# Kernel optimization log

Measured on AMD Instinct MI355X. Metric: run time of the kernel, lower is better.

The kernel has to match this reference:

```python
import jax, jax.numpy as jnp
import numpy as np

B, T, D = 2, 4096, 512
H = 8  # heads; head_dim = D // H = 64


def setup_inputs() -> dict:
    key = jax.random.key(0)
    ks = jax.random.split(key, 8)
    s = 0.02
    return {
        "queries": jax.random.normal(ks[0], (B, T, D), jnp.float32),
        "keys": jax.random.normal(ks[1], (B, T, D), jnp.float32),
        "values": jax.random.normal(ks[2], (B, T, D), jnp.float32),
        "Wq": jax.random.normal(ks[3], (D, D), jnp.float32) * s,
        "Wk": jax.random.normal(ks[4], (D, D), jnp.float32) * s,
        "Wv": jax.random.normal(ks[5], (D, D), jnp.float32) * s,
        "Wo": jax.random.normal(ks[6], (D, D), jnp.float32) * s,
        "bo": jnp.zeros((D,), jnp.float32),
    }


def reference(queries, keys, values, Wq, Wk, Wv, Wo, bo):
    # pad_dim = 0 for in_dim=512, n_heads=8, so no padding needed.
    Bq, Tq, _ = queries.shape
    Ts = keys.shape[1]
    hd = D // H
    # torch Linear: x @ W.T
    q = (queries @ Wq.T).reshape(Bq, Tq, H, hd).transpose(0, 2, 1, 3)  # [B,H,T,hd]
    k = (keys @ Wk.T).reshape(Bq, Ts, H, hd).transpose(0, 2, 1, 3)
    v = (values @ Wv.T).reshape(Bq, Ts, H, hd).transpose(0, 2, 1, 3)
    attn = jnp.einsum("bhtd,bhsd->bhts", q, k) / np.sqrt(hd).astype(np.float32)
    attn = jax.nn.softmax(attn, axis=-1)  # [B,H,T,Ts]
    z = jnp.einsum("bhts,bhsd->bhtd", attn, v)
    z = z.transpose(0, 2, 1, 3).reshape(Bq, Tq, D)
    out = z @ Wo.T + bo
    return (out, attn)
```

## Files before the change

kernel.cpp:

```cpp
#include <hip/hip_runtime.h>

typedef __attribute__((ext_vector_type(8))) short bf16x8;
typedef __attribute__((ext_vector_type(8))) unsigned short u16x8;
typedef __attribute__((ext_vector_type(4))) float f32x4;
typedef __attribute__((ext_vector_type(2))) unsigned uint2v;
typedef __attribute__((ext_vector_type(4))) unsigned uint4v;

#define DEVINL __device__ __forceinline__

constexpr int TB = 2;
constexpr int TT = 4096;
constexpr int TD = 512;
constexpr int TH = 8;
constexpr int THD = 64;
constexpr int TM = TB * TT;

DEVINL unsigned short f2b(float f) {
  unsigned u = __builtin_bit_cast(unsigned, f);
  u += 0x7FFFu + ((u >> 16) & 1u);
  return (unsigned short)(u >> 16);
}

DEVINL unsigned cvtpk(float lo, float hi) {
  unsigned r;
  asm("v_cvt_pk_bf16_f32 %0, %1, %2" : "=v"(r) : "v"(lo), "v"(hi));
  return r;
}

DEVINL void lgkm_barrier() {
  asm volatile("s_waitcnt lgkmcnt(0)" ::: "memory");
  __builtin_amdgcn_s_barrier();
  __builtin_amdgcn_sched_barrier(0);
}

__global__ __launch_bounds__(256, 2)
void proj_qkv(const float* __restrict__ Xq, const float* __restrict__ Xk,
              const float* __restrict__ Xv, const float* __restrict__ Wq,
              const float* __restrict__ Wk, const float* __restrict__ Wv,
              unsigned short* __restrict__ qb, unsigned short* __restrict__ kb,
              unsigned short* __restrict__ vt)
{
  constexpr int K = TD, N = TD;
  __shared__ unsigned short As[128][72];
  __shared__ unsigned short Bs[128][72];

  const int z = blockIdx.z;
  const float* X = (z == 0) ? Xq : (z == 1) ? Xk : Xv;
  const float* W = (z == 0) ? Wq : (z == 1) ? Wk : Wv;
  unsigned short* Yb = (z == 0) ? qb : (z == 1) ? kb : vt;
  const bool TR = (z == 2);

  const int t    = threadIdx.x;
  const int lane = t & 63, w = t >> 6;
  const int fr = lane & 15, fq = lane >> 4;
  const int wr = (w >> 1) * 64, wc = (w & 1) * 64;
  const int bm = blockIdx.x * 128, bn = blockIdx.y * 128;
  const int srow = t >> 1;
  const int skh  = (t & 1) * 32;

  f32x4 acc[4][4];
  #pragma unroll
  for (int i = 0; i < 4; ++i)
    #pragma unroll
    for (int j = 0; j < 4; ++j)
      acc[i][j] = f32x4{0.f, 0.f, 0.f, 0.f};

  for (int k0 = 0; k0 < K; k0 += 64) {
    const float* srcA = X + (size_t)(bm + srow) * K + k0 + skh;
    const float* srcB = W + (size_t)(bn + srow) * K + k0 + skh;
    #pragma unroll
    for (int i = 0; i < 4; ++i) {
      float4 a0 = ((const float4*)srcA)[2 * i];
      float4 a1 = ((const float4*)srcA)[2 * i + 1];
      u16x8 oa = {f2b(a0.x), f2b(a0.y), f2b(a0.z), f2b(a0.w),
                  f2b(a1.x), f2b(a1.y), f2b(a1.z), f2b(a1.w)};
      *(u16x8*)&As[srow][skh + i * 8] = oa;
      float4 b0 = ((const float4*)srcB)[2 * i];
      float4 b1 = ((const float4*)srcB)[2 * i + 1];
      u16x8 ob = {f2b(b0.x), f2b(b0.y), f2b(b0.z), f2b(b0.w),
                  f2b(b1.x), f2b(b1.y), f2b(b1.z), f2b(b1.w)};
      *(u16x8*)&Bs[srow][skh + i * 8] = ob;
    }
    __syncthreads();
    #pragma unroll
    for (int kk = 0; kk < 2; ++kk) {
      bf16x8 af[4], bfv[4];
      #pragma unroll
      for (int i = 0; i < 4; ++i)
        af[i] = *(const bf16x8*)&As[wr + i * 16 + fr][kk * 32 + fq * 8];
      #pragma unroll
      for (int j = 0; j < 4; ++j)
        bfv[j] = *(const bf16x8*)&Bs[wc + j * 16 + fr][kk * 32 + fq * 8];
      if (TR) {
        #pragma unroll
        for (int i = 0; i < 4; ++i)
          #pragma unroll
          for (int j = 0; j < 4; ++j)
            acc[i][j] = __builtin_amdgcn_mfma_f32_16x16x32_bf16(bfv[i], af[j], acc[i][j], 0, 0, 0);
      } else {
        #pragma unroll
        for (int i = 0; i < 4; ++i)
          #pragma unroll
          for (int j = 0; j < 4; ++j)
            acc[i][j] = __builtin_amdgcn_mfma_f32_16x16x32_bf16(af[i], bfv[j], acc[i][j], 0, 0, 0);
      }
    }
    __syncthreads();
  }

  if (TR) {
    #pragma unroll
    for (int i = 0; i < 4; ++i)
      #pragma unroll
      for (int j = 0; j < 4; ++j)
        #pragma unroll
        for (int ii = 0; ii < 4; ++ii) {
          const int Nidx = bn + wc + i * 16 + fq * 4 + ii;
          const int Midx = bm + wr + j * 16 + fr;
          const int h = Nidx >> 6, dd = Nidx & (THD - 1);
          const int b = Midx >> 12, tt = Midx & (TT - 1);
          Yb[((size_t)(b * TH + h) * THD + dd) * TT + tt] = f2b(acc[i][j][ii]);
        }
  } else {
    #pragma unroll
    for (int i = 0; i < 4; ++i)
      #pragma unroll
      for (int j = 0; j < 4; ++j)
        #pragma unroll
        for (int ii = 0; ii < 4; ++ii) {
          const int gm = bm + wr + i * 16 + fq * 4 + ii;
          const int gn = bn + wc + j * 16 + fr;
          Yb[(size_t)gm * N + gn] = f2b(acc[i][j][ii]);
        }
  }
}

__global__ __launch_bounds__(256, 4)
void attn_pass1(const unsigned short* __restrict__ Qb,
                const unsigned short* __restrict__ Kb,
                const unsigned short* __restrict__ VTg,
                float* __restrict__ Z, float* __restrict__ l2iW)
{
  __shared__ unsigned short Ks[2][32][72];
  __shared__ unsigned short VTs[2][64][40];

  const int t    = threadIdx.x;
  const int lane = t & 63, w = t >> 6;
  const int fr = lane & 15, fq = lane >> 4;

  const int d  = blockIdx.x;
  const int bh = 2 * (d & 7) + ((d >> 3) & 1);
  const int q0 = (d >> 4) * 64;
  const int b  = bh >> 3, h = bh & 7;

  const size_t rowKV  = ((size_t)(b * TT)) * TD + h * THD;
  const size_t vtBase = (size_t)bh * THD * TT;

  const int trK = t >> 3, tcK = (t & 7) * 8;
  const int trV = t >> 2, tcV = (t & 3) * 8;

  auto loadK = [&](int kv0, u16x8& r) {
    r = *(const u16x8*)(Kb + rowKV + (size_t)(kv0 + trK) * TD + tcK);
  };
  auto loadVT = [&](int kv0, u16x8& r) {
    r = *(const u16x8*)(VTg + vtBase + (size_t)trV * TT + kv0 + tcV);
  };
  auto writeK  = [&](int buf, const u16x8& r) { *(u16x8*)&Ks[buf][trK][tcK]  = r; };
  auto writeVT = [&](int buf, const u16x8& r) { *(u16x8*)&VTs[buf][trV][tcV] = r; };

  const unsigned short* qsrc = Qb + ((size_t)(b * TT + q0 + w * 16 + fr)) * TD + h * THD;
  bf16x8 aq[2];
  aq[0] = *(const bf16x8*)(qsrc + fq * 8);
  aq[1] = *(const bf16x8*)(qsrc + 32 + fq * 8);

  constexpr int KVB = 32;
  constexpr int NT = TT / KVB;
  constexpr float K2 = 0.18033688011112042f;

  u16x8 kA, vA, kB, vB;
  {
    u16x8 k0, v0;
    loadK(0, k0); loadVT(0, v0);
    writeK(0, k0); writeVT(0, v0);
    loadK(KVB, kB); loadVT(KVB, vB);
    lgkm_barrier();
  }

  float lsum = 0.f;
  f32x4 accz[4];
  #pragma unroll
  for (int n = 0; n < 4; ++n) accz[n] = f32x4{0.f, 0.f, 0.f, 0.f};

  for (int jp = 0; jp < NT / 2; ++jp) {
    #pragma unroll
    for (int half = 0; half < 2; ++half) {
      const int j = jp * 2 + half;
      const int cur = j & 1;
      if (j + 2 < NT) {
        if (half == 0) { loadK((j + 2) * KVB, kA); loadVT((j + 2) * KVB, vA); }
        else           { loadK((j + 2) * KVB, kB); loadVT((j + 2) * KVB, vB); }
      }
      f32x4 sv[2];
      __builtin_amdgcn_s_setprio(1);
      #pragma unroll
      for (int n = 0; n < 2; ++n) {
        f32x4 s = f32x4{0.f, 0.f, 0.f, 0.f};
        #pragma unroll
        for (int kk = 0; kk < 2; ++kk) {
          bf16x8 ak = *(const bf16x8*)&Ks[cur][n * 16 + fr][kk * 32 + fq * 8];
          s = __builtin_amdgcn_mfma_f32_16x16x32_bf16(ak, aq[kk], s, 0, 0, 0);
        }
        sv[n] = s;
      }
      __builtin_amdgcn_s_setprio(0);
      float p[2][4];
      #pragma unroll
      for (int n = 0; n < 2; ++n)
        #pragma unroll
        for (int i = 0; i < 4; ++i) {
          p[n][i] = __builtin_amdgcn_exp2f(sv[n][i] * K2);
          lsum += p[n][i];
        }
      uint4v pav = {cvtpk(p[0][0], p[0][1]), cvtpk(p[0][2], p[0][3]),
                    cvtpk(p[1][0], p[1][1]), cvtpk(p[1][2], p[1][3])};
      bf16x8 ap = __builtin_bit_cast(bf16x8, pav);
      __builtin_amdgcn_s_setprio(1);
      #pragma unroll
      for (int df = 0; df < 4; ++df) {
        uint2v lo = *(const uint2v*)&VTs[cur][df * 16 + fr][fq * 4];
        uint2v hi = *(const uint2v*)&VTs[cur][df * 16 + fr][16 + fq * 4];
        uint4v bvv = {lo[0], lo[1], hi[0], hi[1]};
        accz[df] = __builtin_amdgcn_mfma_f32_16x16x32_bf16(
            ap, __builtin_bit_cast(bf16x8, bvv), accz[df], 0, 0, 0);
      }
      __builtin_amdgcn_s_setprio(0);
      if (j + 1 < NT) {
        if (half == 0) { writeK(cur ^ 1, kB); writeVT(cur ^ 1, vB); }
        else           { writeK(cur ^ 1, kA); writeVT(cur ^ 1, vA); }
      }
      lgkm_barrier();
    }
  }

  lsum += __shfl_xor(lsum, 16, 64);
  lsum += __shfl_xor(lsum, 32, 64);

  if (fq == 0)
    l2iW[(size_t)bh * TT + q0 + w * 16 + fr] = -__log2f(lsum);

  float rls[4];
  #pragma unroll
  for (int i = 0; i < 4; ++i)
    rls[i] = 1.0f / __shfl(lsum, fq * 4 + i, 64);
  const size_t zbase = ((size_t)(b * TT + q0 + w * 16 + fq * 4)) * TD + h * THD + fr;
  #pragma unroll
  for (int df = 0; df < 4; ++df)
    #pragma unroll
    for (int i = 0; i < 4; ++i)
      Z[zbase + (size_t)i * TD + df * 16] = accz[df][i] * rls[i];
}

__global__ __launch_bounds__(256, 4)
void pass2_gemm(const unsigned short* __restrict__ Qb,
                const unsigned short* __restrict__ Kb,
                const float* __restrict__ l2iW,
                float* __restrict__ attnO,
                const float* __restrict__ Zf,
                const float* __restrict__ Wo,
                const float* __restrict__ bo,
                float* __restrict__ outO)
{
  __shared__ __align__(16) char smem_[27648];

  const int t    = threadIdx.x;
  const int lane = t & 63, w = t >> 6;
  const int fr = lane & 15, fq = lane >> 4;
  const int d  = blockIdx.x;

  if (d < 512) {
    auto GAs = (unsigned short (*)[72])smem_;
    auto GBs = (unsigned short (*)[72])(smem_ + 18432);
    const int gm0 = (d >> 3) * 128, gn0 = (d & 7) * 64;
    const int wr = (w >> 1) * 64, wc = (w & 1) * 32;
    const int srow = t >> 1, skh = (t & 1) * 32;
    const int brow = t >> 2, bkh = (t & 3) * 16;
    f32x4 gacc[4][2];
    #pragma unroll
    for (int i = 0; i < 4; ++i)
      #pragma unroll
      for (int j = 0; j < 2; ++j)
        gacc[i][j] = f32x4{0.f, 0.f, 0.f, 0.f};
    for (int k0 = 0; k0 < TD; k0 += 64) {
      const float* srcA = Zf + (size_t)(gm0 + srow) * TD + k0 + skh;
      #pragma unroll
      for (int i = 0; i < 4; ++i) {
        float4 a0 = ((const float4*)srcA)[2 * i];
        float4 a1 = ((const float4*)srcA)[2 * i + 1];
        u16x8 oa = {f2b(a0.x), f2b(a0.y), f2b(a0.z), f2b(a0.w),
                    f2b(a1.x), f2b(a1.y), f2b(a1.z), f2b(a1.w)};
        *(u16x8*)&GAs[srow][skh + i * 8] = oa;
      }
      const float* srcB = Wo + (size_t)(gn0 + brow) * TD + k0 + bkh;
      #pragma unroll
      for (int i = 0; i < 2; ++i) {
        float4 b0 = ((const float4*)srcB)[2 * i];
        float4 b1 = ((const float4*)srcB)[2 * i + 1];
        u16x8 ob = {f2b(b0.x), f2b(b0.y), f2b(b0.z), f2b(b0.w),
                    f2b(b1.x), f2b(b1.y), f2b(b1.z), f2b(b1.w)};
        *(u16x8*)&GBs[brow][bkh + i * 8] = ob;
      }
      __syncthreads();
      #pragma unroll
      for (int kk = 0; kk < 2; ++kk) {
        bf16x8 af[4], bfv[2];
        #pragma unroll
        for (int i = 0; i < 4; ++i)
          af[i] = *(const bf16x8*)&GAs[wr + i * 16 + fr][kk * 32 + fq * 8];
        #pragma unroll
        for (int j = 0; j < 2; ++j)
          bfv[j] = *(const bf16x8*)&GBs[wc + j * 16 + fr][kk * 32 + fq * 8];
        #pragma unroll
        for (int i = 0; i < 4; ++i)
          #pragma unroll
          for (int j = 0; j < 2; ++j)
            gacc[i][j] = __builtin_amdgcn_mfma_f32_16x16x32_bf16(af[i], bfv[j], gacc[i][j], 0, 0, 0);
      }
      __syncthreads();
    }
    #pragma unroll
    for (int i = 0; i < 4; ++i)
      #pragma unroll
      for (int j = 0; j < 2; ++j)
        #pragma unroll
        for (int ii = 0; ii < 4; ++ii) {
          const int gm = gm0 + wr + i * 16 + fq * 4 + ii;
          const int gn = gn0 + wc + j * 16 + fr;
          outO[(size_t)gm * TD + gn] = gacc[i][j][ii] + bo[gn];
        }
    return;
  }

  const int ds = d - 512;
  const int bh = 2 * (ds & 7) + ((ds >> 3) & 1);
  const int q0 = (ds >> 4) * 64;
  const int b  = bh >> 3, h = bh & 7;

  const size_t rowKV = ((size_t)(b * TT)) * TD + h * THD;

  const unsigned short* qsrc = Qb + ((size_t)(b * TT + q0 + w * 16 + fr)) * TD + h * THD;
  bf16x8 aq0 = *(const bf16x8*)(qsrc + fq * 8);
  bf16x8 aq1 = *(const bf16x8*)(qsrc + 32 + fq * 8);

  const float l2i = l2iW[(size_t)bh * TT + q0 + w * 16 + fr];

  constexpr int KVB = 32;
  constexpr int NT = TT / KVB;
  constexpr float K2 = 0.18033688011112042f;

  const int phase = (37 * ds + 32 * w) & (NT - 1);
  auto PH = [&](int jj) { return (jj + phase) & (NT - 1); };

  const unsigned short* kfb = Kb + rowKV + (size_t)fr * TD + fq * 8;
  auto LD = [&](int j, u16x8* f) {
    const unsigned short* p = kfb + (size_t)(j * KVB) * TD;
    f[0] = *(const u16x8*)(p);
    f[1] = *(const u16x8*)(p + 32);
    f[2] = *(const u16x8*)(p + (size_t)16 * TD);
    f[3] = *(const u16x8*)(p + (size_t)16 * TD + 32);
  };

  float* arow = attnO + ((size_t)bh * TT + q0 + w * 16 + fr) * TT + fq * 4;

#define P2C(JJ, F)                                                             \
  {                                                                            \
    const int j = PH(JJ);                                                      \
    f32x4 s0 = f32x4{0.f, 0.f, 0.f, 0.f}, s1 = f32x4{0.f, 0.f, 0.f, 0.f};      \
    __builtin_amdgcn_s_setprio(1);                                             \
    s0 = __builtin_amdgcn_mfma_f32_16x16x32_bf16(__builtin_bit_cast(bf16x8, F[0]), aq0, s0, 0, 0, 0); \
    s0 = __builtin_amdgcn_mfma_f32_16x16x32_bf16(__builtin_bit_cast(bf16x8, F[1]), aq1, s0, 0, 0, 0); \
    s1 = __builtin_amdgcn_mfma_f32_16x16x32_bf16(__builtin_bit_cast(bf16x8, F[2]), aq0, s1, 0, 0, 0); \
    s1 = __builtin_amdgcn_mfma_f32_16x16x32_bf16(__builtin_bit_cast(bf16x8, F[3]), aq1, s1, 0, 0, 0); \
    __builtin_amdgcn_s_setprio(0);                                             \
    f32x4 pv0 = {__builtin_amdgcn_exp2f(fmaf(s0[0], K2, l2i)),                 \
                 __builtin_amdgcn_exp2f(fmaf(s0[1], K2, l2i)),                 \
                 __builtin_amdgcn_exp2f(fmaf(s0[2], K2, l2i)),                 \
                 __builtin_amdgcn_exp2f(fmaf(s0[3], K2, l2i))};                \
    *(f32x4*)(arow + j * KVB) = pv0;                                           \
    f32x4 pv1 = {__builtin_amdgcn_exp2f(fmaf(s1[0], K2, l2i)),                 \
                 __builtin_amdgcn_exp2f(fmaf(s1[1], K2, l2i)),                 \
                 __builtin_amdgcn_exp2f(fmaf(s1[2], K2, l2i)),                 \
                 __builtin_amdgcn_exp2f(fmaf(s1[3], K2, l2i))};                \
    *(f32x4*)(arow + j * KVB + 16) = pv1;                                      \
  }

  u16x8 fA[4], fB[4];
  LD(PH(0), fA);
  for (int jj = 0; jj < NT; jj += 2) {
    if (jj + 1 < NT) LD(PH(jj + 1), fB);
    P2C(jj, fA)
    if (jj + 2 < NT) LD(PH(jj + 2), fA);
    P2C(jj + 1, fB)
  }
#undef P2C
}

extern "C" void kernel_launch(void* const* d_in, const int* in_sizes, int n_in,
                              void* d_out, int out_size, void* d_ws, size_t ws_size,
                              hipStream_t stream) {
  const float* queries = (const float*)d_in[0];
  const float* keys    = (const float*)d_in[1];
  const float* values  = (const float*)d_in[2];
  const float* Wq = (const float*)d_in[3];
  const float* Wk = (const float*)d_in[4];
  const float* Wv = (const float*)d_in[5];
  const float* Wo = (const float*)d_in[6];
  const float* bo = (const float*)d_in[7];

  float* out  = (float*)d_out;
  float* attn = out + (size_t)TM * TD;

  unsigned short* qb = (unsigned short*)d_ws;
  unsigned short* kb = qb + (size_t)TM * TD;
  unsigned short* vt = kb + (size_t)TM * TD;
  float*          zf = (float*)(vt + (size_t)TM * TD);
  float*          l2iW = zf + (size_t)TM * TD;

  proj_qkv<<<dim3(TM / 128, TD / 128, 3), 256, 0, stream>>>(
      queries, keys, values, Wq, Wk, Wv, qb, kb, vt);

  attn_pass1<<<dim3(1024), 256, 0, stream>>>(qb, kb, vt, zf, l2iW);

  pass2_gemm<<<dim3(1536), 256, 0, stream>>>(qb, kb, l2iW, attn,
                                             zf, Wo, bo, out);
}
```

Measured before the change: 549.5 us.

## Stage K tiles through per-wave LDS with coalesced row loads in pass2

```diff
diff --git a/kernel.cpp b/kernel.cpp
--- a/kernel.cpp
+++ b/kernel.cpp
@@ -270,7 +270,7 @@
                 const float* __restrict__ bo,
                 float* __restrict__ outO)
 {
-  __shared__ __align__(16) char smem_[27648];
+  __shared__ __align__(16) char smem_[36864];
 
   const int t    = threadIdx.x;
   const int lane = t & 63, w = t >> 6;
@@ -340,6 +340,8 @@
     return;
   }
 
+  auto KsW = (unsigned short (*)[2][32][72])smem_;
+
   const int ds = d - 512;
   const int bh = 2 * (ds & 7) + ((ds >> 3) & 1);
   const int q0 = (ds >> 4) * 64;
@@ -348,8 +350,9 @@
   const size_t rowKV = ((size_t)(b * TT)) * TD + h * THD;
 
   const unsigned short* qsrc = Qb + ((size_t)(b * TT + q0 + w * 16 + fr)) * TD + h * THD;
-  bf16x8 aq0 = *(const bf16x8*)(qsrc + fq * 8);
-  bf16x8 aq1 = *(const bf16x8*)(qsrc + 32 + fq * 8);
+  bf16x8 aq[2];
+  aq[0] = *(const bf16x8*)(qsrc + fq * 8);
+  aq[1] = *(const bf16x8*)(qsrc + 32 + fq * 8);
 
   const float l2i = l2iW[(size_t)bh * TT + q0 + w * 16 + fr];
 
@@ -358,50 +361,64 @@
   constexpr float K2 = 0.18033688011112042f;
 
   const int phase = (37 * ds + 32 * w) & (NT - 1);
+  const int prow = lane >> 3, pcol = (lane & 7) * 8;
+
+  u16x8 sA[4], sB[4];
+  auto loadKW = [&](int kvt, u16x8* s) {
+    #pragma unroll
+    for (int i = 0; i < 4; ++i)
+      s[i] = *(const u16x8*)(Kb + rowKV +
+               (size_t)(kvt * KVB + i * 8 + prow) * TD + pcol);
+  };
+  auto writeKW = [&](int buf, const u16x8* s) {
+    #pragma unroll
+    for (int i = 0; i < 4; ++i)
+      *(u16x8*)&KsW[w][buf][i * 8 + prow][pcol] = s[i];
+  };
   auto PH = [&](int jj) { return (jj + phase) & (NT - 1); };
 
-  const unsigned short* kfb = Kb + rowKV + (size_t)fr * TD + fq * 8;
-  auto LD = [&](int j, u16x8* f) {
-    const unsigned short* p = kfb + (size_t)(j * KVB) * TD;
-    f[0] = *(const u16x8*)(p);
-    f[1] = *(const u16x8*)(p + 32);
-    f[2] = *(const u16x8*)(p + (size_t)16 * TD);
-    f[3] = *(const u16x8*)(p + (size_t)16 * TD + 32);
-  };
-
   float* arow = attnO + ((size_t)bh * TT + q0 + w * 16 + fr) * TT + fq * 4;
 
-#define P2C(JJ, F)                                                             \
+#define P2_COMPUTE(JJ, BUF)                                                    \
   {                                                                            \
     const int j = PH(JJ);                                                      \
-    f32x4 s0 = f32x4{0.f, 0.f, 0.f, 0.f}, s1 = f32x4{0.f, 0.f, 0.f, 0.f};      \
+    f32x4 sv[2];                                                               \
     __builtin_amdgcn_s_setprio(1);                                             \
-    s0 = __builtin_amdgcn_mfma_f32_16x16x32_bf16(__builtin_bit_cast(bf16x8, F[0]), aq0, s0, 0, 0, 0); \
-    s0 = __builtin_amdgcn_mfma_f32_16x16x32_bf16(__builtin_bit_cast(bf16x8, F[1]), aq1, s0, 0, 0, 0); \
-    s1 = __builtin_amdgcn_mfma_f32_16x16x32_bf16(__builtin_bit_cast(bf16x8, F[2]), aq0, s1, 0, 0, 0); \
-    s1 = __builtin_amdgcn_mfma_f32_16x16x32_bf16(__builtin_bit_cast(bf16x8, F[3]), aq1, s1, 0, 0, 0); \
+    _Pragma("unroll")                                                          \
+    for (int n = 0; n < 2; ++n) {                                              \
+      f32x4 s = f32x4{0.f, 0.f, 0.f, 0.f};                                     \
+      _Pragma("unroll")                                                        \
+      for (int kk = 0; kk < 2; ++kk) {                                         \
+        bf16x8 ak = *(const bf16x8*)&KsW[w][(BUF)][n * 16 + fr][kk * 32 + fq * 8]; \
+        s = __builtin_amdgcn_mfma_f32_16x16x32_bf16(ak, aq[kk], s, 0, 0, 0);   \
+      }                                                                        \
+      sv[n] = s;                                                               \
+    }                                                                          \
     __builtin_amdgcn_s_setprio(0);                                             \
-    f32x4 pv0 = {__builtin_amdgcn_exp2f(fmaf(s0[0], K2, l2i)),                 \
-                 __builtin_amdgcn_exp2f(fmaf(s0[1], K2, l2i)),                 \
-                 __builtin_amdgcn_exp2f(fmaf(s0[2], K2, l2i)),                 \
-                 __builtin_amdgcn_exp2f(fmaf(s0[3], K2, l2i))};                \
-    *(f32x4*)(arow + j * KVB) = pv0;                                           \
-    f32x4 pv1 = {__builtin_amdgcn_exp2f(fmaf(s1[0], K2, l2i)),                 \
-                 __builtin_amdgcn_exp2f(fmaf(s1[1], K2, l2i)),                 \
-                 __builtin_amdgcn_exp2f(fmaf(s1[2], K2, l2i)),                 \
-                 __builtin_amdgcn_exp2f(fmaf(s1[3], K2, l2i))};                \
-    *(f32x4*)(arow + j * KVB + 16) = pv1;                                      \
-  }
-
-  u16x8 fA[4], fB[4];
-  LD(PH(0), fA);
-  for (int jj = 0; jj < NT; jj += 2) {
-    if (jj + 1 < NT) LD(PH(jj + 1), fB);
-    P2C(jj, fA)
-    if (jj + 2 < NT) LD(PH(jj + 2), fA);
-    P2C(jj + 1, fB)
-  }
-#undef P2C
+    _Pragma("unroll")                                                          \
+    for (int n = 0; n < 2; ++n) {                                              \
+      f32x4 pv4 = {__builtin_amdgcn_exp2f(fmaf(sv[n][0], K2, l2i)),            \
+                   __builtin_amdgcn_exp2f(fmaf(sv[n][1], K2, l2i)),            \
+                   __builtin_amdgcn_exp2f(fmaf(sv[n][2], K2, l2i)),            \
+                   __builtin_amdgcn_exp2f(fmaf(sv[n][3], K2, l2i))};           \
+      *(f32x4*)(arow + j * KVB + n * 16) = pv4;                                \
+    }                                                                          \
+  }
+
+  loadKW(PH(0), sA);
+  writeKW(0, sA);
+  loadKW(PH(1), sB);
+
+  for (int jp = 0; jp < NT / 2; ++jp) {
+    const int jj0 = 2 * jp;
+    if (jj0 + 2 < NT) loadKW(PH(jj0 + 2), sA);
+    P2_COMPUTE(jj0, 0)
+    writeKW(1, sB);
+    if (jj0 + 3 < NT) loadKW(PH(jj0 + 3), sB);
+    P2_COMPUTE(jj0 + 1, 1)
+    if (jj0 + 2 < NT) writeKW(0, sA);
+  }
+#undef P2_COMPUTE
 }
 
 extern "C" void kernel_launch(void* const* d_in, const int* in_sizes, int n_in,
```

Measured after the change: 492.6 us. 1.12x faster.
